# Kernel optimization log

Measured on AMD Instinct MI355X. Metric: run time of the kernel, lower is better.

Reference implementation:

```python
import jax, jax.numpy as jnp
import numpy as np
from functools import partial

N = 9
NN = N * N  # 81 cells
BTS = 4096
HID = 100


def build_constraint_mask():
    idx = np.arange(NN)
    r, c = idx // N, idx % N
    b = (r // 3) * 3 + (c // 3)
    row = (r[:, None] == r[None, :]).astype(np.float32)
    col = (c[:, None] == c[None, :]).astype(np.float32)
    box = (b[:, None] == b[None, :]).astype(np.float32)
    return jnp.asarray(np.stack([row, col, box], axis=1))  # [81, 3, 81]


def setup_inputs() -> dict:
    key = jax.random.key(0)
    k1, k2, k3, k4 = jax.random.split(key, 4)
    vals = jax.random.randint(k1, (BTS, NN), 0, N)
    filled = jax.random.uniform(k2, (BTS, NN)) < 0.4
    x = jax.nn.one_hot(vals, N, dtype=jnp.float32) * filled[:, :, None].astype(jnp.float32)
    W1 = jax.random.normal(k3, (HID, 3 * N), dtype=jnp.float32) * 0.1
    W2 = jax.random.normal(k4, (N, HID), dtype=jnp.float32) * 0.1
    return {"x": x, "W1": W1, "W2": W2, "constraint_mask": build_constraint_mask()}


def _sudoku_forward(x, W1, W2, cmask):
    bts = x.shape[0]
    b_idx = jnp.arange(bts)

    def step(carry, _):
        x, x_pred = carry
        # constraints[b,i,k,v] = sum_j cmask[i,k,j] * x[b,j,v]  -> [b,81,3,9]
        constraints = jnp.einsum('ikj,bjv->bikv', cmask, x)
        f = constraints.reshape(bts, NN, 3 * N)            # [b,81,27]
        h = jax.nn.relu(jnp.einsum('bif,hf->bih', f, W1))  # [b,81,100]
        y = jnp.einsum('bih,vh->biv', h, W2)               # [b,81,9]
        probs = jax.nn.softmax(y, axis=-1)
        empty = x.sum(-1) == 0                             # [b,81]
        x_pred = jnp.where(empty[..., None], probs, x_pred)
        s = jnp.where(empty[..., None], probs, 0.0)
        score = s.max(-1)                                  # [b,81]
        pos = jnp.argmax(s, -1)                            # [b,81]
        mmax = jnp.argmax(score, -1)                       # [b] best cell
        has_empty = empty.any(-1)                          # [b]
        sel_pos = pos[b_idx, mmax]
        newv = jnp.where(has_empty, 1.0, x[b_idx, mmax, sel_pos])
        x = x.at[b_idx, mmax, sel_pos].set(newv)
        return (x, x_pred), None

    # Original loops min_empty (max empties over batch) times; running the full
    # NN=81 steps is equivalent since iterations past a board's fill are no-ops.
    (x, x_pred), _ = jax.lax.scan(step, (x, x), None, length=NN)
    return x_pred, x


@jax.jit
def reference(x, W1, W2, constraint_mask):
    return _sudoku_forward(x, W1, W2, constraint_mask)
```

## Files before the change

### kernel.cpp

```cpp
#include <hip/hip_runtime.h>

#define TPB 256


__device__ __forceinline__ int affected_cell(int slot, int fr, int fc) {
    if (slot < 9)  return fr * 9 + slot;
    if (slot < 18) return (slot - 9) * 9 + fc;
    int r0 = (fr / 3) * 3, c0 = (fc / 3) * 3;
    int dr = fr - r0, dc = fc - c0;
    int rA = r0 + (dr == 0 ? 1 : 0), rB = r0 + (dr == 2 ? 1 : 2);
    int cA = c0 + (dc == 0 ? 1 : 0), cB = c0 + (dc == 2 ? 1 : 2);
    int k = slot - 18;
    return ((k < 2) ? rA : rB) * 9 + ((k & 1) ? cB : cA);
}

__device__ __forceinline__ void do_FC(int slot, int qv, int cell,
    const double* __restrict__ H1, const double* __restrict__ W2Td,
    double* __restrict__ pbuf, double* __restrict__ ybuf,
    float* __restrict__ outp, double* __restrict__ score_l, int* __restrict__ pos_l)
{
    int r = cell / 9, c = cell - 9 * r;
    int bx = (r / 3) * 3 + c / 3;
    const double* Hr = H1 + r * 101;
    const double* Hc = H1 + (9 + c) * 101;
    const double* Hb = H1 + (18 + bx) * 101;
    double acc[9];
#pragma unroll
    for (int v = 0; v < 9; v++) acc[v] = 0.0;
    const int j0 = qv * 12;
#pragma unroll
    for (int jj = 0; jj < 12; jj++) {
        int j = j0 + jj;
        if (j < 100) {
            double h = Hr[j] + Hc[j] + Hb[j];
            h = h > 0.0 ? h : 0.0;
            const double* w = W2Td + j * 9;
#pragma unroll
            for (int v = 0; v < 9; v++) acc[v] = fma(h, w[v], acc[v]);
        }
    }
    double* pb = pbuf + (slot * 9 + qv) * 9;
#pragma unroll
    for (int v = 0; v < 9; v++) pb[v] = acc[v];
    __builtin_amdgcn_wave_barrier();
    double y = 0.0;
#pragma unroll
    for (int q2 = 0; q2 < 9; q2++) y += pbuf[(slot * 9 + q2) * 9 + qv];
    ybuf[slot * 9 + qv] = y;
    __builtin_amdgcn_wave_barrier();
    double m = ybuf[slot * 9 + 0];
#pragma unroll
    for (int v2 = 1; v2 < 9; v2++) m = fmax(m, ybuf[slot * 9 + v2]);
    double e = exp(y - m);
    __builtin_amdgcn_wave_barrier();
    ybuf[slot * 9 + qv] = e;
    __builtin_amdgcn_wave_barrier();
    double p[9], sum = 0.0;
#pragma unroll
    for (int v2 = 0; v2 < 9; v2++) { p[v2] = ybuf[slot * 9 + v2]; sum += p[v2]; }
    double inv = 1.0 / sum;
    outp[cell * 9 + qv] = (float)(p[qv] * inv);
    if (qv == 0) {
        double best = -1.0; int bvv = 0;
#pragma unroll
        for (int v2 = 0; v2 < 9; v2++) {
            double pr = p[v2] * inv;
            if (pr > best) { best = pr; bvv = v2; }
        }
        score_l[cell] = best;
        pos_l[cell] = bvv;
    }
}

__global__ __launch_bounds__(TPB, 3) void sudoku_kernel(
    const float* __restrict__ x_in,
    const float* __restrict__ W1,
    const float* __restrict__ W2,
    float* __restrict__ out,
    int nb)
{
    const int b = blockIdx.x;
    const int t = threadIdx.x;
    const int W = t >> 6, l = t & 63;
    const int ls = l / 9, qv = l - 9 * ls;

    __shared__ float  xs[729];
    __shared__ double W2Td[100 * 9];
    __shared__ double cnt[27 * 9];
    __shared__ double H1[27 * 101];
    __shared__ double pbuf[24 * 81];
    __shared__ double ybuf[24 * 9];
    __shared__ double score_l[81];
    __shared__ int    pos_l[81];

    float* outp = out + (size_t)b * 729;
    const float* xb = x_in + (size_t)b * 729;
    for (int i = t; i < 729; i += TPB) { float v = xb[i]; xs[i] = v; outp[i] = v; }
    for (int i = t; i < 900; i += TPB) { int v = i / 100, j = i - 100 * v; W2Td[j * 9 + v] = (double)W2[i]; }
    __syncthreads();

    if (t < 81) {
        float s = 0.f;
#pragma unroll
        for (int v = 0; v < 9; v++) s += xs[t * 9 + v];
        score_l[t] = (s == 0.f) ? 0.0 : -1.0;
        pos_l[t] = 0;
    }
    for (int o = t; o < 243; o += TPB) {
        int g = o / 9, v = o - 9 * g;
        float s = 0.f;
        if (g < 9) {
            int base = g * 9;
#pragma unroll
            for (int k = 0; k < 9; k++) s += xs[(base + k) * 9 + v];
        } else if (g < 18) {
            int c = g - 9;
#pragma unroll
            for (int k = 0; k < 9; k++) s += xs[(c + 9 * k) * 9 + v];
        } else {
            int bx = g - 18;
            int base = (bx / 3) * 27 + (bx % 3) * 3;
#pragma unroll
            for (int k = 0; k < 9; k++) s += xs[(base + (k / 3) * 9 + (k % 3)) * 9 + v];
        }
        cnt[g * 9 + v] = (double)s;
    }
    __syncthreads();

    for (int o = t; o < 2700; o += TPB) {
        int g = o / 100, j = o - 100 * g;
        int type = (g >= 18) ? 2 : (g >= 9 ? 1 : 0);
        const float* w = W1 + j * 27 + type * 9;
        const double* cc = cnt + g * 9;
        double s = 0.0;
#pragma unroll
        for (int v = 0; v < 9; v++) s = fma((double)w[v], cc[v], s);
        H1[g * 101 + j] = s;
    }
    int myflag = (t < 81) ? (score_l[t] == 0.0) : 0;
    int ne = __syncthreads_count(myflag);

    for (int c0 = 0; c0 < 96; c0 += 24) {
        if (l < 54) {
            int slot = W * 6 + ls;
            int cell = c0 + slot;
            if (cell < 81 && score_l[cell] >= 0.0)
                do_FC(slot, qv, cell, H1, W2Td, pbuf, ybuf, outp, score_l, pos_l);
        }
    }
    __syncthreads();

    for (int step = 0; step < ne; ++step) {
        double s = score_l[l]; int idx = l;
        if (l < 17) {
            double s2 = score_l[64 + l];
            if (s2 > s) { s = s2; idx = 64 + l; }
        }
#pragma unroll
        for (int off = 1; off < 64; off <<= 1) {
            double s2 = __shfl_xor(s, off);
            int    i2 = __shfl_xor(idx, off);
            if (s2 > s || (s2 == s && i2 < idx)) { s = s2; idx = i2; }
        }
        const int fcell = idx;
        const int bv = pos_l[fcell];
        const int fr = fcell / 9, fcc = fcell - 9 * fr;
        const int fbx = (fr / 3) * 3 + fcc / 3;

        for (int o = t; o < 300; o += TPB) {
            int gi = o / 100, j = o - 100 * gi;
            int g = (gi == 0) ? fr : (gi == 1) ? (9 + fcc) : (18 + fbx);
            const float* w = W1 + j * 27 + gi * 9;
            const double* cc = cnt + g * 9;
            double h = 0.0;
#pragma unroll
            for (int v = 0; v < 9; v++) {
                double cv = cc[v] + (v == bv ? 1.0 : 0.0);
                h = fma((double)w[v], cv, h);
            }
            H1[g * 101 + j] = h;
        }
        __syncthreads();

        if (t == 0) {
            xs[fcell * 9 + bv] = 1.0f;
            score_l[fcell] = -1.0;
            cnt[fr * 9 + bv] += 1.0;
            cnt[(9 + fcc) * 9 + bv] += 1.0;
            cnt[(18 + fbx) * 9 + bv] += 1.0;
        }
        if (l < 54) {
            int slot = W * 6 + ls;
            if (slot < 22) {
                int cell = affected_cell(slot, fr, fcc);
                if (cell != fcell && score_l[cell] >= 0.0)
                    do_FC(slot, qv, cell, H1, W2Td, pbuf, ybuf, outp, score_l, pos_l);
            }
        }
        __syncthreads();
    }

    float* outx = out + (size_t)nb * 729 + (size_t)b * 729;
    for (int i = t; i < 729; i += TPB) outx[i] = xs[i];
}

extern "C" void kernel_launch(void* const* d_in, const int* in_sizes, int n_in,
                              void* d_out, int out_size, void* d_ws, size_t ws_size,
                              hipStream_t stream) {
    const float* x  = (const float*)d_in[0];
    const float* W1 = (const float*)d_in[1];
    const float* W2 = (const float*)d_in[2];
    int nb = in_sizes[0] / 729;
    (void)n_in; (void)out_size; (void)d_ws; (void)ws_size;
    sudoku_kernel<<<nb, TPB, 0, stream>>>(x, W1, W2, (float*)d_out, nb);
}
```

Before: 1.338 ms.

## Run each board with a single wavefront to drop block barriers

Each board now runs in one 64-thread wavefront instead of a 256-thread block. Every __syncthreads becomes a wave barrier, and the per-cell FC work is split across 22 slots by 5 hidden-chunks, with softmax done in registers over several rounds. W1 rows for the incremental H1 update are cached in registers, and the count table moves to float. Outputs are written directly instead of being staged in shared memory. This removes block-wide synchronisation on the long serial step loop and raises occupancy, but each step now has less parallel width and runs more serial work per lane.

```diff
diff --git a/kernel.cpp b/kernel.cpp
--- a/kernel.cpp
+++ b/kernel.cpp
@@ -1,6 +1,4 @@
 #include <hip/hip_runtime.h>
-
-#define TPB 256
 
 
 __device__ __forceinline__ int affected_cell(int slot, int fr, int fc) {
@@ -14,65 +12,105 @@
     return ((k < 2) ? rA : rB) * 9 + ((k & 1) ? cB : cA);
 }
 
-__device__ __forceinline__ void do_FC(int slot, int qv, int cell,
-    const double* __restrict__ H1, const double* __restrict__ W2Td,
-    double* __restrict__ pbuf, double* __restrict__ ybuf,
-    float* __restrict__ outp, double* __restrict__ score_l, int* __restrict__ pos_l)
+__device__ __forceinline__ void fc_pass(int c0, int fr, int fc, int l,
+    const double* H1, double* pbuf, double* ybuf,
+    double* score_l, int* pos_l, const double* W2Td, float* outp)
 {
-    int r = cell / 9, c = cell - 9 * r;
-    int bx = (r / 3) * 3 + c / 3;
-    const double* Hr = H1 + r * 101;
-    const double* Hc = H1 + (9 + c) * 101;
-    const double* Hb = H1 + (18 + bx) * 101;
-    double acc[9];
-#pragma unroll
-    for (int v = 0; v < 9; v++) acc[v] = 0.0;
-    const int j0 = qv * 12;
-#pragma unroll
-    for (int jj = 0; jj < 12; jj++) {
-        int j = j0 + jj;
-        if (j < 100) {
-            double h = Hr[j] + Hc[j] + Hb[j];
-            h = h > 0.0 ? h : 0.0;
-            const double* w = W2Td + j * 9;
-#pragma unroll
-            for (int v = 0; v < 9; v++) acc[v] = fma(h, w[v], acc[v]);
-        }
-    }
-    double* pb = pbuf + (slot * 9 + qv) * 9;
-#pragma unroll
-    for (int v = 0; v < 9; v++) pb[v] = acc[v];
-    __builtin_amdgcn_wave_barrier();
-    double y = 0.0;
-#pragma unroll
-    for (int q2 = 0; q2 < 9; q2++) y += pbuf[(slot * 9 + q2) * 9 + qv];
-    ybuf[slot * 9 + qv] = y;
-    __builtin_amdgcn_wave_barrier();
-    double m = ybuf[slot * 9 + 0];
-#pragma unroll
-    for (int v2 = 1; v2 < 9; v2++) m = fmax(m, ybuf[slot * 9 + v2]);
-    double e = exp(y - m);
-    __builtin_amdgcn_wave_barrier();
-    ybuf[slot * 9 + qv] = e;
-    __builtin_amdgcn_wave_barrier();
-    double p[9], sum = 0.0;
-#pragma unroll
-    for (int v2 = 0; v2 < 9; v2++) { p[v2] = ybuf[slot * 9 + v2]; sum += p[v2]; }
-    double inv = 1.0 / sum;
-    outp[cell * 9 + qv] = (float)(p[qv] * inv);
-    if (qv == 0) {
-        double best = -1.0; int bvv = 0;
-#pragma unroll
-        for (int v2 = 0; v2 < 9; v2++) {
-            double pr = p[v2] * inv;
-            if (pr > best) { best = pr; bvv = v2; }
-        }
-        score_l[cell] = best;
-        pos_l[cell] = bvv;
-    }
-}
-
-__global__ __launch_bounds__(TPB, 3) void sudoku_kernel(
+#pragma unroll
+    for (int r = 0; r < 2; r++) {
+        int u = r * 64 + l;
+        if (u < 110) {
+            int slot = u % 22, q = u / 22;
+            int cell = (c0 >= 0) ? ((c0 + slot < 81) ? c0 + slot : -1)
+                                 : affected_cell(slot, fr, fc);
+            if (cell >= 0 && score_l[cell] >= 0.0) {
+                int rr = cell / 9, cc = cell - 9 * rr;
+                int bx = (rr / 3) * 3 + cc / 3;
+                const double* Hr = H1 + rr * 102;
+                const double* Hc = H1 + (9 + cc) * 102;
+                const double* Hb = H1 + (18 + bx) * 102;
+                double acc[9];
+#pragma unroll
+                for (int v = 0; v < 9; v++) acc[v] = 0.0;
+                const int j0 = q * 20;
+#pragma unroll
+                for (int jj = 0; jj < 20; jj++) {
+                    int j = j0 + jj;
+                    double h = Hr[j] + Hc[j] + Hb[j];
+                    h = h > 0.0 ? h : 0.0;
+                    const double* w = W2Td + j * 9;
+#pragma unroll
+                    for (int v = 0; v < 9; v++) acc[v] = fma(h, w[v], acc[v]);
+                }
+                double* pb = pbuf + (slot * 5 + q) * 9;
+#pragma unroll
+                for (int v = 0; v < 9; v++) pb[v] = acc[v];
+            }
+        }
+    }
+    __builtin_amdgcn_wave_barrier();
+    double yreg[4], ereg[4];
+    int ucell[4], uslot[4], uv[4];
+#pragma unroll
+    for (int r = 0; r < 4; r++) {
+        int u = r * 64 + l;
+        int slot = 0, v = 0, cell = -1;
+        if (u < 198) {
+            slot = u % 22; v = u / 22;
+            cell = (c0 >= 0) ? ((c0 + slot < 81) ? c0 + slot : -1)
+                             : affected_cell(slot, fr, fc);
+            if (cell >= 0 && score_l[cell] < 0.0) cell = -1;
+        }
+        double y = 0.0;
+        if (cell >= 0) {
+#pragma unroll
+            for (int q = 0; q < 5; q++) y += pbuf[(slot * 5 + q) * 9 + v];
+            ybuf[slot * 9 + v] = y;
+        }
+        yreg[r] = y; ucell[r] = cell; uslot[r] = slot; uv[r] = v;
+    }
+    __builtin_amdgcn_wave_barrier();
+#pragma unroll
+    for (int r = 0; r < 4; r++) {
+        ereg[r] = 0.0;
+        if (ucell[r] >= 0) {
+            int slot = uslot[r];
+            double m = ybuf[slot * 9 + 0];
+#pragma unroll
+            for (int v2 = 1; v2 < 9; v2++) m = fmax(m, ybuf[slot * 9 + v2]);
+            ereg[r] = exp(yreg[r] - m);
+        }
+    }
+    __builtin_amdgcn_wave_barrier();
+#pragma unroll
+    for (int r = 0; r < 4; r++)
+        if (ucell[r] >= 0) pbuf[uslot[r] * 9 + uv[r]] = ereg[r];
+    __builtin_amdgcn_wave_barrier();
+#pragma unroll
+    for (int r = 0; r < 4; r++) {
+        if (ucell[r] >= 0) {
+            int slot = uslot[r], v = uv[r], cell = ucell[r];
+            double ee[9], sum = 0.0;
+#pragma unroll
+            for (int v2 = 0; v2 < 9; v2++) { ee[v2] = pbuf[slot * 9 + v2]; sum += ee[v2]; }
+            double inv = 1.0 / sum;
+            outp[cell * 9 + v] = (float)(ereg[r] * inv);
+            if (v == 0) {
+                double best = -1.0; int bp = 0;
+#pragma unroll
+                for (int v2 = 0; v2 < 9; v2++) {
+                    double pr = ee[v2] * inv;
+                    if (pr > best) { best = pr; bp = v2; }
+                }
+                score_l[cell] = best;
+                pos_l[cell] = bp;
+            }
+        }
+    }
+    __builtin_amdgcn_wave_barrier();
+}
+
+__global__ __launch_bounds__(64) void sudoku_kernel(
     const float* __restrict__ x_in,
     const float* __restrict__ W1,
     const float* __restrict__ W2,
@@ -80,75 +118,94 @@
     int nb)
 {
     const int b = blockIdx.x;
-    const int t = threadIdx.x;
-    const int W = t >> 6, l = t & 63;
-    const int ls = l / 9, qv = l - 9 * ls;
-
-    __shared__ float  xs[729];
-    __shared__ double W2Td[100 * 9];
-    __shared__ double cnt[27 * 9];
-    __shared__ double H1[27 * 101];
-    __shared__ double pbuf[24 * 81];
-    __shared__ double ybuf[24 * 9];
+    const int l = threadIdx.x;
+
+    __shared__ double H1[27 * 102];
+    __shared__ double pbuf[990];
+    __shared__ double W2Td[900];
+    __shared__ double ybuf[198];
     __shared__ double score_l[81];
+    __shared__ float  cnt[243];
     __shared__ int    pos_l[81];
 
+    const float* xb = x_in + (size_t)b * 729;
     float* outp = out + (size_t)b * 729;
-    const float* xb = x_in + (size_t)b * 729;
-    for (int i = t; i < 729; i += TPB) { float v = xb[i]; xs[i] = v; outp[i] = v; }
-    for (int i = t; i < 900; i += TPB) { int v = i / 100, j = i - 100 * v; W2Td[j * 9 + v] = (double)W2[i]; }
-    __syncthreads();
-
-    if (t < 81) {
-        float s = 0.f;
-#pragma unroll
-        for (int v = 0; v < 9; v++) s += xs[t * 9 + v];
-        score_l[t] = (s == 0.f) ? 0.0 : -1.0;
-        pos_l[t] = 0;
-    }
-    for (int o = t; o < 243; o += TPB) {
-        int g = o / 9, v = o - 9 * g;
-        float s = 0.f;
-        if (g < 9) {
-            int base = g * 9;
-#pragma unroll
-            for (int k = 0; k < 9; k++) s += xs[(base + k) * 9 + v];
-        } else if (g < 18) {
-            int c = g - 9;
-#pragma unroll
-            for (int k = 0; k < 9; k++) s += xs[(c + 9 * k) * 9 + v];
-        } else {
-            int bx = g - 18;
-            int base = (bx / 3) * 27 + (bx % 3) * 3;
-#pragma unroll
-            for (int k = 0; k < 9; k++) s += xs[(base + (k / 3) * 9 + (k % 3)) * 9 + v];
-        }
-        cnt[g * 9 + v] = (double)s;
-    }
-    __syncthreads();
-
-    for (int o = t; o < 2700; o += TPB) {
-        int g = o / 100, j = o - 100 * g;
-        int type = (g >= 18) ? 2 : (g >= 9 ? 1 : 0);
-        const float* w = W1 + j * 27 + type * 9;
-        const double* cc = cnt + g * 9;
-        double s = 0.0;
-#pragma unroll
-        for (int v = 0; v < 9; v++) s = fma((double)w[v], cc[v], s);
-        H1[g * 101 + j] = s;
-    }
-    int myflag = (t < 81) ? (score_l[t] == 0.0) : 0;
-    int ne = __syncthreads_count(myflag);
-
-    for (int c0 = 0; c0 < 96; c0 += 24) {
-        if (l < 54) {
-            int slot = W * 6 + ls;
-            int cell = c0 + slot;
-            if (cell < 81 && score_l[cell] >= 0.0)
-                do_FC(slot, qv, cell, H1, W2Td, pbuf, ybuf, outp, score_l, pos_l);
-        }
-    }
-    __syncthreads();
+    float* outx = out + (size_t)nb * 729 + (size_t)b * 729;
+
+#pragma unroll
+    for (int r = 0; r < 12; r++) {
+        int i = r * 64 + l;
+        if (i < 729) { float v = xb[i]; outp[i] = v; outx[i] = v; }
+    }
+#pragma unroll
+    for (int r = 0; r < 15; r++) {
+        int i = r * 64 + l;
+        if (i < 900) { int v = i / 100, j = i - 100 * v; W2Td[j * 9 + v] = (double)W2[i]; }
+    }
+#pragma unroll
+    for (int r = 0; r < 2; r++) {
+        int u = r * 64 + l;
+        if (u < 81) {
+            float s = 0.f;
+#pragma unroll
+            for (int v = 0; v < 9; v++) s += xb[u * 9 + v];
+            score_l[u] = (s == 0.f) ? 0.0 : -1.0;
+            pos_l[u] = 0;
+        }
+    }
+#pragma unroll
+    for (int r = 0; r < 4; r++) {
+        int o = r * 64 + l;
+        if (o < 243) {
+            int g = o / 9, v = o - 9 * g;
+            float s = 0.f;
+            if (g < 9) {
+                int base = g * 9;
+#pragma unroll
+                for (int k = 0; k < 9; k++) s += xb[(base + k) * 9 + v];
+            } else if (g < 18) {
+                int c = g - 9;
+#pragma unroll
+                for (int k = 0; k < 9; k++) s += xb[(c + 9 * k) * 9 + v];
+            } else {
+                int bx = g - 18;
+                int base = (bx / 3) * 27 + (bx % 3) * 3;
+#pragma unroll
+                for (int k = 0; k < 9; k++) s += xb[(base + (k / 3) * 9 + (k % 3)) * 9 + v];
+            }
+            cnt[o] = s;
+        }
+    }
+    __builtin_amdgcn_wave_barrier();
+    for (int r = 0; r < 43; r++) {
+        int o = r * 64 + l;
+        if (o < 2700) {
+            int g = o / 100, j = o - 100 * g;
+            int type = (g >= 18) ? 2 : (g >= 9 ? 1 : 0);
+            const float* w = W1 + j * 27 + type * 9;
+            double s = 0.0;
+#pragma unroll
+            for (int v = 0; v < 9; v++) s = fma((double)w[v], (double)cnt[g * 9 + v], s);
+            H1[g * 102 + j] = s;
+        }
+    }
+    float w1r[5][9];
+#pragma unroll
+    for (int k = 0; k < 5; k++) {
+        int o = k * 64 + l; if (o >= 300) o = 0;
+        int gi = o / 100, j = o - 100 * gi;
+#pragma unroll
+        for (int v = 0; v < 9; v++) w1r[k][v] = W1[j * 27 + gi * 9 + v];
+    }
+    __builtin_amdgcn_wave_barrier();
+
+    fc_pass(0,  0, 0, l, H1, pbuf, ybuf, score_l, pos_l, W2Td, outp);
+    fc_pass(22, 0, 0, l, H1, pbuf, ybuf, score_l, pos_l, W2Td, outp);
+    fc_pass(44, 0, 0, l, H1, pbuf, ybuf, score_l, pos_l, W2Td, outp);
+    fc_pass(66, 0, 0, l, H1, pbuf, ybuf, score_l, pos_l, W2Td, outp);
+
+    int ne = __popcll(__ballot(score_l[l] >= 0.0));
+    ne += __popcll(__ballot(l < 17 && score_l[64 + l] >= 0.0));
 
     for (int step = 0; step < ne; ++step) {
         double s = score_l[l]; int idx = l;
@@ -164,44 +221,32 @@
         }
         const int fcell = idx;
         const int bv = pos_l[fcell];
-        const int fr = fcell / 9, fcc = fcell - 9 * fr;
-        const int fbx = (fr / 3) * 3 + fcc / 3;
-
-        for (int o = t; o < 300; o += TPB) {
-            int gi = o / 100, j = o - 100 * gi;
-            int g = (gi == 0) ? fr : (gi == 1) ? (9 + fcc) : (18 + fbx);
-            const float* w = W1 + j * 27 + gi * 9;
-            const double* cc = cnt + g * 9;
-            double h = 0.0;
-#pragma unroll
-            for (int v = 0; v < 9; v++) {
-                double cv = cc[v] + (v == bv ? 1.0 : 0.0);
-                h = fma((double)w[v], cv, h);
-            }
-            H1[g * 101 + j] = h;
-        }
-        __syncthreads();
-
-        if (t == 0) {
-            xs[fcell * 9 + bv] = 1.0f;
+        const int fr = fcell / 9, fc = fcell - 9 * fr;
+        const int fbx = (fr / 3) * 3 + fc / 3;
+        if (l == 0) {
             score_l[fcell] = -1.0;
-            cnt[fr * 9 + bv] += 1.0;
-            cnt[(9 + fcc) * 9 + bv] += 1.0;
-            cnt[(18 + fbx) * 9 + bv] += 1.0;
-        }
-        if (l < 54) {
-            int slot = W * 6 + ls;
-            if (slot < 22) {
-                int cell = affected_cell(slot, fr, fcc);
-                if (cell != fcell && score_l[cell] >= 0.0)
-                    do_FC(slot, qv, cell, H1, W2Td, pbuf, ybuf, outp, score_l, pos_l);
-            }
-        }
-        __syncthreads();
-    }
-
-    float* outx = out + (size_t)nb * 729 + (size_t)b * 729;
-    for (int i = t; i < 729; i += TPB) outx[i] = xs[i];
+            cnt[fr * 9 + bv] += 1.f;
+            cnt[(9 + fc) * 9 + bv] += 1.f;
+            cnt[(18 + fbx) * 9 + bv] += 1.f;
+            outx[fcell * 9 + bv] = 1.0f;
+        }
+        __builtin_amdgcn_wave_barrier();
+#pragma unroll
+        for (int k = 0; k < 5; k++) {
+            int o = k * 64 + l;
+            if (o < 300) {
+                int gi = o / 100, j = o - 100 * gi;
+                int g = (gi == 0) ? fr : (gi == 1) ? (9 + fc) : (18 + fbx);
+                double h = 0.0;
+#pragma unroll
+                for (int v = 0; v < 9; v++)
+                    h = fma((double)w1r[k][v], (double)cnt[g * 9 + v], h);
+                H1[g * 102 + j] = h;
+            }
+        }
+        __builtin_amdgcn_wave_barrier();
+        fc_pass(-1, fr, fc, l, H1, pbuf, ybuf, score_l, pos_l, W2Td, outp);
+    }
 }
 
 extern "C" void kernel_launch(void* const* d_in, const int* in_sizes, int n_in,
@@ -212,5 +257,5 @@
     const float* W2 = (const float*)d_in[2];
     int nb = in_sizes[0] / 729;
     (void)n_in; (void)out_size; (void)d_ws; (void)ws_size;
-    sudoku_kernel<<<nb, TPB, 0, stream>>>(x, W1, W2, (float*)d_out, nb);
-}
+    sudoku_kernel<<<nb, 64, 0, stream>>>(x, W1, W2, (float*)d_out, nb);
+}
```

Result: slower. 2.750 ms (+105.5%).

## Replicate counts per wave and double-buffer scores to drop one barrier per step

Applied to the files above, without the earlier changes.

Each wave now keeps its own byte-sized copy of the row/column/box counts and recomputes the affected H1 rows redundantly, so the per-step H1 update only needs a wave barrier instead of a block barrier. Scores are double-buffered (scur/snext) so the FC pass can read old scores while writing new ones, leaving one __syncthreads per step. The FC pass is regrouped to 5 lanes per cell with 20 hidden units each, and the softmax uses shuffles instead of shared-memory round trips. Shared memory shrinks, launch bounds rise to 4 blocks, and the xs board copy is replaced by writing x directly to the output. The price is redundant H1 work in every wave and extra register pressure from the shuffle-based softmax.

```diff
diff --git a/kernel.cpp b/kernel.cpp
--- a/kernel.cpp
+++ b/kernel.cpp
@@ -14,65 +14,78 @@
     return ((k < 2) ? rA : rB) * 9 + ((k & 1) ? cB : cA);
 }
 
-__device__ __forceinline__ void do_FC(int slot, int qv, int cell,
+__device__ __forceinline__ void fc_pass(int c0, int fcell, int fr, int fcol,
+    int l, int slotBase,
     const double* __restrict__ H1, const double* __restrict__ W2Td,
-    double* __restrict__ pbuf, double* __restrict__ ybuf,
-    float* __restrict__ outp, double* __restrict__ score_l, int* __restrict__ pos_l)
+    double* __restrict__ pbuf, const double* __restrict__ scur,
+    double* __restrict__ snext, int* __restrict__ pos_l,
+    float* __restrict__ outp)
 {
-    int r = cell / 9, c = cell - 9 * r;
-    int bx = (r / 3) * 3 + c / 3;
-    const double* Hr = H1 + r * 101;
-    const double* Hc = H1 + (9 + c) * 101;
-    const double* Hb = H1 + (18 + bx) * 101;
-    double acc[9];
-#pragma unroll
-    for (int v = 0; v < 9; v++) acc[v] = 0.0;
-    const int j0 = qv * 12;
-#pragma unroll
-    for (int jj = 0; jj < 12; jj++) {
-        int j = j0 + jj;
-        if (j < 100) {
-            double h = Hr[j] + Hc[j] + Hb[j];
-            h = h > 0.0 ? h : 0.0;
-            const double* w = W2Td + j * 9;
-#pragma unroll
-            for (int v = 0; v < 9; v++) acc[v] = fma(h, w[v], acc[v]);
-        }
-    }
-    double* pb = pbuf + (slot * 9 + qv) * 9;
-#pragma unroll
-    for (int v = 0; v < 9; v++) pb[v] = acc[v];
+    if (l < 30) {
+        int ls = l / 5, q = l - 5 * ls;
+        int slot = slotBase + ls;
+        if (slot < 22) {
+            int cell = (c0 >= 0) ? (c0 + slot) : affected_cell(slot, fr, fcol);
+            if (cell < 81 && cell != fcell && scur[cell] >= 0.0) {
+                int rr = cell / 9, cc = cell - 9 * rr;
+                int bx = (rr / 3) * 3 + cc / 3;
+                const double* Hr = H1 + rr * 101;
+                const double* Hc = H1 + (9 + cc) * 101;
+                const double* Hb = H1 + (18 + bx) * 101;
+                double acc[9];
+#pragma unroll
+                for (int v = 0; v < 9; v++) acc[v] = 0.0;
+                const int j0 = q * 20;
+#pragma unroll 4
+                for (int jj = 0; jj < 20; jj++) {
+                    int j = j0 + jj;
+                    double h = Hr[j] + Hc[j] + Hb[j];
+                    h = h > 0.0 ? h : 0.0;
+                    const double* w = W2Td + j * 9;
+#pragma unroll
+                    for (int v = 0; v < 9; v++) acc[v] = fma(h, w[v], acc[v]);
+                }
+                double* pb = pbuf + (slot * 5 + q) * 9;
+#pragma unroll
+                for (int v = 0; v < 9; v++) pb[v] = acc[v];
+            }
+        }
+    }
     __builtin_amdgcn_wave_barrier();
-    double y = 0.0;
-#pragma unroll
-    for (int q2 = 0; q2 < 9; q2++) y += pbuf[(slot * 9 + q2) * 9 + qv];
-    ybuf[slot * 9 + qv] = y;
+    if (l < 54) {
+        int ls = l / 9, v = l - 9 * ls;
+        int slot = slotBase + ls;
+        if (slot < 22) {
+            int cell = (c0 >= 0) ? (c0 + slot) : affected_cell(slot, fr, fcol);
+            if (cell < 81 && cell != fcell && scur[cell] >= 0.0) {
+                double y = 0.0;
+#pragma unroll
+                for (int q2 = 0; q2 < 5; q2++) y += pbuf[(slot * 5 + q2) * 9 + v];
+                const int base = ls * 9;
+                double m = __shfl(y, base);
+#pragma unroll
+                for (int k = 1; k < 9; k++) m = fmax(m, __shfl(y, base + k));
+                double e = exp(y - m);
+                double sum = 0.0;
+#pragma unroll
+                for (int k = 0; k < 9; k++) sum += __shfl(e, base + k);
+                double inv = 1.0 / sum;
+                double pr = e * inv;
+                outp[cell * 9 + v] = (float)pr;
+                double best = -1.0; int bp = 0;
+#pragma unroll
+                for (int k = 0; k < 9; k++) {
+                    double pk = __shfl(pr, base + k);
+                    if (pk > best) { best = pk; bp = k; }
+                }
+                if (v == 0) { snext[cell] = best; pos_l[cell] = bp; }
+            }
+        }
+    }
     __builtin_amdgcn_wave_barrier();
-    double m = ybuf[slot * 9 + 0];
-#pragma unroll
-    for (int v2 = 1; v2 < 9; v2++) m = fmax(m, ybuf[slot * 9 + v2]);
-    double e = exp(y - m);
-    __builtin_amdgcn_wave_barrier();
-    ybuf[slot * 9 + qv] = e;
-    __builtin_amdgcn_wave_barrier();
-    double p[9], sum = 0.0;
-#pragma unroll
-    for (int v2 = 0; v2 < 9; v2++) { p[v2] = ybuf[slot * 9 + v2]; sum += p[v2]; }
-    double inv = 1.0 / sum;
-    outp[cell * 9 + qv] = (float)(p[qv] * inv);
-    if (qv == 0) {
-        double best = -1.0; int bvv = 0;
-#pragma unroll
-        for (int v2 = 0; v2 < 9; v2++) {
-            double pr = p[v2] * inv;
-            if (pr > best) { best = pr; bvv = v2; }
-        }
-        score_l[cell] = best;
-        pos_l[cell] = bvv;
-    }
-}
-
-__global__ __launch_bounds__(TPB, 3) void sudoku_kernel(
+}
+
+__global__ __launch_bounds__(TPB, 4) void sudoku_kernel(
     const float* __restrict__ x_in,
     const float* __restrict__ W1,
     const float* __restrict__ W2,
@@ -82,78 +95,85 @@
     const int b = blockIdx.x;
     const int t = threadIdx.x;
     const int W = t >> 6, l = t & 63;
-    const int ls = l / 9, qv = l - 9 * ls;
-
-    __shared__ float  xs[729];
+    const int slotBase = W * 6;
+
+    __shared__ double H1[27 * 101];
     __shared__ double W2Td[100 * 9];
-    __shared__ double cnt[27 * 9];
-    __shared__ double H1[27 * 101];
-    __shared__ double pbuf[24 * 81];
-    __shared__ double ybuf[24 * 9];
-    __shared__ double score_l[81];
+    __shared__ double pbuf[22 * 5 * 9];
+    __shared__ double sb0[81], sb1[81];
     __shared__ int    pos_l[81];
-
+    __shared__ unsigned char cntw[4 * 244];
+
+    const float* xb = x_in + (size_t)b * 729;
     float* outp = out + (size_t)b * 729;
-    const float* xb = x_in + (size_t)b * 729;
-    for (int i = t; i < 729; i += TPB) { float v = xb[i]; xs[i] = v; outp[i] = v; }
-    for (int i = t; i < 900; i += TPB) { int v = i / 100, j = i - 100 * v; W2Td[j * 9 + v] = (double)W2[i]; }
-    __syncthreads();
-
+    float* outx = out + (size_t)nb * 729 + (size_t)b * 729;
+
+    for (int i = t; i < 729; i += TPB) { float v = xb[i]; outp[i] = v; outx[i] = v; }
+    for (int i = t; i < 900; i += TPB) {
+        int v = i / 100, j = i - 100 * v;
+        W2Td[j * 9 + v] = (double)W2[i];
+    }
     if (t < 81) {
         float s = 0.f;
 #pragma unroll
-        for (int v = 0; v < 9; v++) s += xs[t * 9 + v];
-        score_l[t] = (s == 0.f) ? 0.0 : -1.0;
+        for (int v = 0; v < 9; v++) s += xb[t * 9 + v];
+        sb0[t] = (s == 0.f) ? 0.0 : -1.0;
         pos_l[t] = 0;
     }
-    for (int o = t; o < 243; o += TPB) {
-        int g = o / 9, v = o - 9 * g;
-        float s = 0.f;
-        if (g < 9) {
-            int base = g * 9;
-#pragma unroll
-            for (int k = 0; k < 9; k++) s += xs[(base + k) * 9 + v];
-        } else if (g < 18) {
-            int c = g - 9;
-#pragma unroll
-            for (int k = 0; k < 9; k++) s += xs[(c + 9 * k) * 9 + v];
-        } else {
-            int bx = g - 18;
-            int base = (bx / 3) * 27 + (bx % 3) * 3;
-#pragma unroll
-            for (int k = 0; k < 9; k++) s += xs[(base + (k / 3) * 9 + (k % 3)) * 9 + v];
-        }
-        cnt[g * 9 + v] = (double)s;
+    unsigned char* cw = cntw + W * 244;
+#pragma unroll
+    for (int r = 0; r < 4; r++) {
+        int o = r * 64 + l;
+        if (o < 243) {
+            int g = o / 9, v = o - 9 * g;
+            float s = 0.f;
+            if (g < 9) {
+                int base = g * 9;
+#pragma unroll
+                for (int k = 0; k < 9; k++) s += xb[(base + k) * 9 + v];
+            } else if (g < 18) {
+                int c = g - 9;
+#pragma unroll
+                for (int k = 0; k < 9; k++) s += xb[(c + 9 * k) * 9 + v];
+            } else {
+                int bx = g - 18;
+                int base = (bx / 3) * 27 + (bx % 3) * 3;
+#pragma unroll
+                for (int k = 0; k < 9; k++) s += xb[(base + (k / 3) * 9 + (k % 3)) * 9 + v];
+            }
+            cw[o] = (unsigned char)(int)s;
+        }
+    }
+    __builtin_amdgcn_wave_barrier();
+    for (int r = 0; r < 43; r++) {
+        int o = r * 64 + l;
+        if (o < 2700) {
+            int g = o / 100, j = o - 100 * g;
+            int type = (g >= 18) ? 2 : (g >= 9 ? 1 : 0);
+            const float* w = W1 + j * 27 + type * 9;
+            const unsigned char* cg = cw + g * 9;
+            double s = 0.0;
+#pragma unroll
+            for (int v = 0; v < 9; v++) s = fma((double)w[v], (double)cg[v], s);
+            H1[g * 101 + j] = s;
+        }
     }
     __syncthreads();
 
-    for (int o = t; o < 2700; o += TPB) {
-        int g = o / 100, j = o - 100 * g;
-        int type = (g >= 18) ? 2 : (g >= 9 ? 1 : 0);
-        const float* w = W1 + j * 27 + type * 9;
-        const double* cc = cnt + g * 9;
-        double s = 0.0;
-#pragma unroll
-        for (int v = 0; v < 9; v++) s = fma((double)w[v], cc[v], s);
-        H1[g * 101 + j] = s;
-    }
-    int myflag = (t < 81) ? (score_l[t] == 0.0) : 0;
-    int ne = __syncthreads_count(myflag);
-
-    for (int c0 = 0; c0 < 96; c0 += 24) {
-        if (l < 54) {
-            int slot = W * 6 + ls;
-            int cell = c0 + slot;
-            if (cell < 81 && score_l[cell] >= 0.0)
-                do_FC(slot, qv, cell, H1, W2Td, pbuf, ybuf, outp, score_l, pos_l);
-        }
-    }
+    for (int p = 0; p < 4; p++)
+        fc_pass(p * 22, -1, 0, 0, l, slotBase, H1, W2Td, pbuf, sb0, sb0, pos_l, outp);
     __syncthreads();
 
+    int ne = __popcll(__ballot(sb0[l] >= 0.0));
+    ne += __popcll(__ballot((l < 17) && (sb0[64 + l] >= 0.0)));
+
+    double* scur = sb0;
+    double* snext = sb1;
+
     for (int step = 0; step < ne; ++step) {
-        double s = score_l[l]; int idx = l;
+        double s = scur[l]; int idx = l;
         if (l < 17) {
-            double s2 = score_l[64 + l];
+            double s2 = scur[64 + l];
             if (s2 > s) { s = s2; idx = 64 + l; }
         }
 #pragma unroll
@@ -164,44 +184,46 @@
         }
         const int fcell = idx;
         const int bv = pos_l[fcell];
-        const int fr = fcell / 9, fcc = fcell - 9 * fr;
-        const int fbx = (fr / 3) * 3 + fcc / 3;
-
-        for (int o = t; o < 300; o += TPB) {
-            int gi = o / 100, j = o - 100 * gi;
-            int g = (gi == 0) ? fr : (gi == 1) ? (9 + fcc) : (18 + fbx);
-            const float* w = W1 + j * 27 + gi * 9;
-            const double* cc = cnt + g * 9;
-            double h = 0.0;
-#pragma unroll
-            for (int v = 0; v < 9; v++) {
-                double cv = cc[v] + (v == bv ? 1.0 : 0.0);
-                h = fma((double)w[v], cv, h);
-            }
-            H1[g * 101 + j] = h;
+        const int frow = fcell / 9, fcol = fcell - 9 * frow;
+        const int fbx = (frow / 3) * 3 + fcol / 3;
+
+        if (t == 0) outx[fcell * 9 + bv] = 1.0f;
+        if (l == 0) {
+            cw[frow * 9 + bv] += 1;
+            cw[(9 + fcol) * 9 + bv] += 1;
+            cw[(18 + fbx) * 9 + bv] += 1;
+        }
+        __builtin_amdgcn_wave_barrier();
+
+#pragma unroll
+        for (int k = 0; k < 5; k++) {
+            int o = k * 64 + l;
+            if (o < 300) {
+                int gi = o / 100, j = o - 100 * gi;
+                int g = (gi == 0) ? frow : (gi == 1) ? (9 + fcol) : (18 + fbx);
+                const float* w = W1 + j * 27 + gi * 9;
+                const unsigned char* cg = cw + g * 9;
+                double h = 0.0;
+#pragma unroll
+                for (int v = 0; v < 9; v++) h = fma((double)w[v], (double)cg[v], h);
+                H1[g * 101 + j] = h;
+            }
+        }
+        __builtin_amdgcn_wave_barrier();
+
+        fc_pass(-1, fcell, frow, fcol, l, slotBase, H1, W2Td, pbuf, scur, snext, pos_l, outp);
+
+        if (t < 81) {
+            int cr = t / 9, cc = t - 9 * cr;
+            bool aff = (cr == frow) || (cc == fcol) ||
+                       ((cr / 3) == (frow / 3) && (cc / 3) == (fcol / 3));
+            double sc = scur[t];
+            if (t == fcell) snext[t] = -1.0;
+            else if (!(aff && sc >= 0.0)) snext[t] = sc;
         }
         __syncthreads();
-
-        if (t == 0) {
-            xs[fcell * 9 + bv] = 1.0f;
-            score_l[fcell] = -1.0;
-            cnt[fr * 9 + bv] += 1.0;
-            cnt[(9 + fcc) * 9 + bv] += 1.0;
-            cnt[(18 + fbx) * 9 + bv] += 1.0;
-        }
-        if (l < 54) {
-            int slot = W * 6 + ls;
-            if (slot < 22) {
-                int cell = affected_cell(slot, fr, fcc);
-                if (cell != fcell && score_l[cell] >= 0.0)
-                    do_FC(slot, qv, cell, H1, W2Td, pbuf, ybuf, outp, score_l, pos_l);
-            }
-        }
-        __syncthreads();
-    }
-
-    float* outx = out + (size_t)nb * 729 + (size_t)b * 729;
-    for (int i = t; i < 729; i += TPB) outx[i] = xs[i];
+        double* tmp = scur; scur = snext; snext = tmp;
+    }
 }
 
 extern "C" void kernel_launch(void* const* d_in, const int* in_sizes, int n_in,
```

After: 2.669 ms. 1.99x slower.
